# Kernel optimization log

Hardware: AMD Instinct MI355X
Metric: run time of the kernel (lower is better)

Reference implementation:

```python
import jax, jax.numpy as jnp
import numpy as np

D = 512; H = 8; DH = 64; FF = 2048; NL = 4
CB = 8; V = 2048
NFFT = 1280; HOP = 320; WIN = 1280; SWIN = 30; UP = 6
B = 2; T = 256


def setup_inputs() -> dict:
    key = jax.random.key(0)
    ks = jax.random.split(key, 12)
    s = 0.02
    return {
        "codes": jax.random.randint(ks[0], (B, CB, T), 0, V),
        "emb": jax.random.normal(ks[1], (CB * V, D), jnp.float32) * s,
        "ln1": jnp.ones((NL, D), jnp.float32),
        "ln2": jnp.ones((NL, D), jnp.float32),
        "fln": jnp.ones((D,), jnp.float32),
        "wq": jax.random.normal(ks[2], (NL, D, D), jnp.float32) * s,
        "wk": jax.random.normal(ks[3], (NL, D, D), jnp.float32) * s,
        "wv": jax.random.normal(ks[4], (NL, D, D), jnp.float32) * s,
        "wo": jax.random.normal(ks[5], (NL, D, D), jnp.float32) * s,
        "wg": jax.random.normal(ks[6], (NL, D, FF), jnp.float32) * s,
        "wu": jax.random.normal(ks[7], (NL, D, FF), jnp.float32) * s,
        "wd": jax.random.normal(ks[8], (NL, FF, D), jnp.float32) * s,
        "lin_w": jax.random.normal(ks[9], (D, 1282), jnp.float32) * s,
        "lin_b": jnp.zeros((1282,), jnp.float32),
    }


def _rmsnorm(x, w):
    return x * jax.lax.rsqrt(jnp.mean(x * x, axis=-1, keepdims=True) + 1e-5) * w


def _forward(codes, emb, ln1, ln2, fln, wq, wk, wv, wo, wg, wu, wd, lin_w, lin_b):
    b, c, t = codes.shape
    # FusedEmbedding: offset per codebook, lookup, mean over codebooks -> [B,T,D]
    ids = codes + (jnp.arange(c) * V)[None, :, None]
    x = emb[ids].mean(axis=1)
    x = jnp.repeat(x, UP, axis=1)  # [B,S,D]
    S = x.shape[1]
    idx = jnp.arange(S)
    d = idx[None, :] - idx[:, None]
    mask = (d <= 0) & (d > -SWIN)  # [S,S] causal sliding-window band
    scale = float(1.0 / np.sqrt(DH))
    for l in range(NL):
        h = _rmsnorm(x, ln1[l])
        q = (h @ wq[l]).reshape(b, S, H, DH)
        k = (h @ wk[l]).reshape(b, S, H, DH)
        v = (h @ wv[l]).reshape(b, S, H, DH)
        sc = jnp.einsum('bqhd,bkhd->bhqk', q, k) * scale
        sc = jnp.where(mask[None, None], sc, jnp.float32(-1e30))
        a = jax.nn.softmax(sc, axis=-1)
        o = jnp.einsum('bhqk,bkhd->bqhd', a, v).reshape(b, S, D) @ wo[l]
        x = x + o
        h = _rmsnorm(x, ln2[l])
        x = x + (jax.nn.silu(h @ wg[l]) * (h @ wu[l])) @ wd[l]
    x = _rmsnorm(x, fln)
    x = x @ lin_w + lin_b            # [B,S,1282]
    x = jnp.swapaxes(x, 1, 2)        # [B,1282,S]
    log_abs, angle = jnp.split(x, 2, axis=1)  # [B,641,S] each
    mag = jnp.exp(log_abs)
    spec = jax.lax.complex(mag * jnp.cos(angle), mag * jnp.sin(angle))
    # ISTFT with 'same' padding (Vocos-style overlap-add)
    ifft = jnp.fft.irfft(spec, n=NFFT, axis=1)               # [B,NFFT,S]
    n = jnp.arange(WIN, dtype=jnp.float32)
    win = 0.5 * (1.0 - jnp.cos(2.0 * jnp.pi * n / WIN))      # periodic hann
    ifft = ifft * win[None, :, None]
    out_size = (S - 1) * HOP + WIN
    pos = (jnp.arange(S)[:, None] * HOP + jnp.arange(WIN)[None, :]).reshape(-1)
    frames = jnp.swapaxes(ifft, 1, 2).reshape(b, -1)
    y = jnp.zeros((b, out_size), ifft.dtype).at[:, pos].add(frames)
    env = jnp.zeros((out_size,), jnp.float32).at[pos].add(jnp.tile(win * win, S))
    pad = (WIN - HOP) // 2
    return y[:, pad:-pad] / env[pad:-pad]


def reference(codes, emb, ln1, ln2, fln, wq, wk, wv, wo, wg, wu, wd, lin_w, lin_b):
    return _forward(codes, emb, ln1, ln2, fln, wq, wk, wv, wo, wg, wu, wd, lin_w, lin_b)
```

## Files before the change

### kernel.cpp

```cpp
#include <hip/hip_runtime.h>
#include <math.h>

#define B_    2
#define T_    256
#define S_    1536
#define D_    512
#define H_    8
#define DH_   64
#define FF_   2048
#define V_    2048
#define NL_   4
#define NFFT_ 1280
#define HOP_  320
#define WIN_  1280
#define NBIN_ 641
#define NC_   1282
#define NPADL 1344
#define PAD_  480
#define OUTL_ 491520
#define SWIN_ 30
#define ROW_  (B_ * S_)
#define NH_   641
#define KH_   704
#define NHP_  704

#define TWO_PI_OVER_N 0.004908738521234052f

typedef unsigned short ushort_t;
typedef __attribute__((ext_vector_type(8))) short short8;
typedef __attribute__((ext_vector_type(8))) unsigned short ushort8_t;
typedef __attribute__((ext_vector_type(4))) float f32x4;

__device__ __forceinline__ ushort_t f2bf(float x) {
    unsigned int u = __builtin_bit_cast(unsigned int, x);
    u = (u + 0x7fffu + ((u >> 16) & 1u)) >> 16;
    return (ushort_t)u;
}
__device__ __forceinline__ float bf2f(ushort_t h) {
    unsigned int u = ((unsigned int)h) << 16;
    return __builtin_bit_cast(float, u);
}

#define GLL16(gp, sp) \
    __builtin_amdgcn_global_load_lds((const __attribute__((address_space(1))) void*)(gp), \
                                     (__attribute__((address_space(3))) void*)(sp), 16, 0, 0)

__device__ __forceinline__ int soff64(int r) {
    return r * 128;
}

__global__ __launch_bounds__(256) void k_embed(const int* __restrict__ codes,
                                               const float* __restrict__ emb,
                                               float* __restrict__ X)
{
    int idx = blockIdx.x * 256 + threadIdx.x;
    int d  = idx & (D_ - 1);
    int bt = idx >> 9;
    int t  = bt & (T_ - 1);
    int b  = bt >> 8;
    float s = 0.f;
#pragma unroll
    for (int cb = 0; cb < 8; ++cb) {
        int code = codes[(b * 8 + cb) * T_ + t];
        s += emb[(size_t)(cb * V_ + code) * D_ + d];
    }
    s *= 0.125f;
    float* xp = X + (size_t)(b * S_ + t * 6) * D_ + d;
#pragma unroll
    for (int r = 0; r < 6; ++r) xp[(size_t)r * D_] = s;
}

__global__ __launch_bounds__(256) void k_rmsnorm(const float* __restrict__ X,
                                                 const float* __restrict__ w,
                                                 ushort_t* __restrict__ Hh,
                                                 ushort_t* __restrict__ Hl)
{
    int row = blockIdx.x;
    int tid = threadIdx.x;
    const float* x = X + (size_t)row * D_;
    float v0 = x[tid], v1 = x[tid + 256];
    float ss = v0 * v0 + v1 * v1;
#pragma unroll
    for (int m = 1; m < 64; m <<= 1) ss += __shfl_xor(ss, m);
    __shared__ float red[4];
    if ((tid & 63) == 0) red[tid >> 6] = ss;
    __syncthreads();
    float tot = red[0] + red[1] + red[2] + red[3];
    float sc = rsqrtf(tot * (1.f / (float)D_) + 1e-5f);
    float y0 = v0 * sc * w[tid];
    float y1 = v1 * sc * w[tid + 256];
    ushort_t h0 = f2bf(y0), h1 = f2bf(y1);
    Hh[(size_t)row * D_ + tid]       = h0;
    Hh[(size_t)row * D_ + tid + 256] = h1;
    if (Hl) {
        Hl[(size_t)row * D_ + tid]       = f2bf(y0 - bf2f(h0));
        Hl[(size_t)row * D_ + tid + 256] = f2bf(y1 - bf2f(h1));
    }
}

__global__ __launch_bounds__(256) void k_castT(const float* __restrict__ src,
                                               ushort_t* __restrict__ dh,
                                               ushort_t* __restrict__ dl,
                                               int K, int N,
                                               long srcBatchStride, long dstBatchStride)
{
    src += (size_t)blockIdx.z * srcBatchStride;
    dh  += (size_t)blockIdx.z * dstBatchStride;
    if (dl) dl += (size_t)blockIdx.z * dstBatchStride;
    __shared__ float t[32][33];
    int n0 = blockIdx.x * 32, k0 = blockIdx.y * 32;
    int tx = threadIdx.x & 31, ty = threadIdx.x >> 5;
#pragma unroll
    for (int i = 0; i < 4; ++i) {
        int k = k0 + ty + 8 * i, n = n0 + tx;
        t[ty + 8 * i][tx] = (n < N) ? src[(size_t)k * N + n] : 0.f;
    }
    __syncthreads();
#pragma unroll
    for (int i = 0; i < 4; ++i) {
        int n = n0 + ty + 8 * i;
        float v = t[tx][ty + 8 * i];
        ushort_t h = f2bf(v);
        dh[(size_t)n * K + k0 + tx] = h;
        if (dl) dl[(size_t)n * K + k0 + tx] = f2bf(v - bf2f(h));
    }
}

template<bool SPLIT, bool CBF16, bool HASRES, bool HASBIAS>
__global__ __launch_bounds__(256) void gemm_mfma(
    const ushort_t* __restrict__ Ah, const ushort_t* __restrict__ Al,
    const ushort_t* __restrict__ Bh, const ushort_t* __restrict__ Bl,
    const float* __restrict__ Res, const float* __restrict__ bias,
    float* __restrict__ Cf, ushort_t* __restrict__ Cb,
    int K, int Nstore, size_t az, size_t bz, size_t cz)
{
    const size_t zo = blockIdx.z;
    Ah += zo * az; Bh += zo * bz;
    if (SPLIT) { Al += zo * az; Bl += zo * bz; }
    if (CBF16) Cb += zo * cz; else Cf += zo * cz;

    const int f  = blockIdx.y * gridDim.x + blockIdx.x;
    const int tx = f / gridDim.y;
    const int ty = f - tx * gridDim.y;

    __shared__ __align__(16) ushort_t lds[SPLIT ? 16384 : 8192];
    ushort_t* AsH = lds;
    ushort_t* BsH = lds + 4096;

    const int tid  = threadIdx.x;
    const int wave = tid >> 6, lane = tid & 63;
    const int row0 = ty * 64;
    const int col0 = tx * 64;
    const int wr = (wave >> 1) * 32, wc = (wave & 1) * 32;

    const int sr0 = tid >> 3, js = tid & 7;
    const int sr1 = 32 + sr0;
    const int jg0 = (js - (sr0 >> 1)) & 7;
    const int jg1 = (js - (sr1 >> 1)) & 7;
    const size_t aSrc0 = (size_t)(row0 + sr0) * K + jg0 * 8;
    const size_t aSrc1 = (size_t)(row0 + sr1) * K + jg1 * 8;
    const size_t bSrc0 = (size_t)(col0 + sr0) * K + jg0 * 8;
    const size_t bSrc1 = (size_t)(col0 + sr1) * K + jg1 * 8;
    const int d0 = tid * 16, d1 = d0 + 4096;

    const int kg = lane >> 4;
    const int lr = lane & 15;
    const int rA0 = wr + lr,      rA1 = wr + 16 + lr;
    const int rB0 = wc + lr,      rB1 = wc + 16 + lr;
    const int offA0 = rA0 * 128 + (((kg + (rA0 >> 1)) & 7) * 16);
    const int offA1 = rA1 * 128 + (((kg + (rA1 >> 1)) & 7) * 16);
    const int offB0 = rB0 * 128 + (((kg + (rB0 >> 1)) & 7) * 16);
    const int offB1 = rB1 * 128 + (((kg + (rB1 >> 1)) & 7) * 16);

    f32x4 acc00 = {0.f,0.f,0.f,0.f}, acc01 = acc00, acc10 = acc00, acc11 = acc00;

    for (int k0 = 0; k0 < K; k0 += 64) {
        GLL16(Ah + aSrc0 + k0, (char*)AsH + d0);
        GLL16(Ah + aSrc1 + k0, (char*)AsH + d1);
        GLL16(Bh + bSrc0 + k0, (char*)BsH + d0);
        GLL16(Bh + bSrc1 + k0, (char*)BsH + d1);
        if constexpr (SPLIT) {
            GLL16(Al + aSrc0 + k0, (char*)(lds + 8192)  + d0);
            GLL16(Al + aSrc1 + k0, (char*)(lds + 8192)  + d1);
            GLL16(Bl + bSrc0 + k0, (char*)(lds + 12288) + d0);
            GLL16(Bl + bSrc1 + k0, (char*)(lds + 12288) + d1);
        }
        __syncthreads();
#pragma unroll
        for (int h = 0; h < 2; ++h) {
            const int hx = h * 64;
            short8 a0 = *(const short8*)((const char*)AsH + (offA0 ^ hx));
            short8 a1 = *(const short8*)((const char*)AsH + (offA1 ^ hx));
            short8 b0 = *(const short8*)((const char*)BsH + (offB0 ^ hx));
            short8 b1 = *(const short8*)((const char*)BsH + (offB1 ^ hx));
            acc00 = __builtin_amdgcn_mfma_f32_16x16x32_bf16(a0, b0, acc00, 0, 0, 0);
            acc01 = __builtin_amdgcn_mfma_f32_16x16x32_bf16(a0, b1, acc01, 0, 0, 0);
            acc10 = __builtin_amdgcn_mfma_f32_16x16x32_bf16(a1, b0, acc10, 0, 0, 0);
            acc11 = __builtin_amdgcn_mfma_f32_16x16x32_bf16(a1, b1, acc11, 0, 0, 0);
            if constexpr (SPLIT) {
                short8 al0 = *(const short8*)((const char*)(lds + 8192)  + (offA0 ^ hx));
                short8 al1 = *(const short8*)((const char*)(lds + 8192)  + (offA1 ^ hx));
                short8 bl0 = *(const short8*)((const char*)(lds + 12288) + (offB0 ^ hx));
                short8 bl1 = *(const short8*)((const char*)(lds + 12288) + (offB1 ^ hx));
                acc00 = __builtin_amdgcn_mfma_f32_16x16x32_bf16(a0, bl0, acc00, 0, 0, 0);
                acc00 = __builtin_amdgcn_mfma_f32_16x16x32_bf16(al0, b0, acc00, 0, 0, 0);
                acc01 = __builtin_amdgcn_mfma_f32_16x16x32_bf16(a0, bl1, acc01, 0, 0, 0);
                acc01 = __builtin_amdgcn_mfma_f32_16x16x32_bf16(al0, b1, acc01, 0, 0, 0);
                acc10 = __builtin_amdgcn_mfma_f32_16x16x32_bf16(a1, bl0, acc10, 0, 0, 0);
                acc10 = __builtin_amdgcn_mfma_f32_16x16x32_bf16(al1, b0, acc10, 0, 0, 0);
                acc11 = __builtin_amdgcn_mfma_f32_16x16x32_bf16(a1, bl1, acc11, 0, 0, 0);
                acc11 = __builtin_amdgcn_mfma_f32_16x16x32_bf16(al1, b1, acc11, 0, 0, 0);
            }
        }
        __syncthreads();
    }

    const int crow = row0 + wr + (lane >> 4) * 4;
    const int ccol = col0 + wc + lr;
#pragma unroll
    for (int i = 0; i < 2; ++i) {
#pragma unroll
        for (int j = 0; j < 2; ++j) {
            const f32x4 a = (i == 0) ? (j == 0 ? acc00 : acc01) : (j == 0 ? acc10 : acc11);
            int c = ccol + j * 16;
            if (c >= Nstore) continue;
            float bi = HASBIAS ? bias[c] : 0.f;
#pragma unroll
            for (int r = 0; r < 4; ++r) {
                int rr = crow + i * 16 + r;
                float v = a[r] + bi;
                if (HASRES) v += Res[(size_t)rr * Nstore + c];
                if (CBF16) Cb[(size_t)rr * Nstore + c] = f2bf(v);
                else       Cf[(size_t)rr * Nstore + c] = v;
            }
        }
    }
}

__global__ __launch_bounds__(256) void gemm_swiglu(
    const ushort_t* __restrict__ Ah,
    const ushort_t* __restrict__ Bg, const ushort_t* __restrict__ Bu,
    ushort_t* __restrict__ F, int K)
{
    const int f  = blockIdx.y * gridDim.x + blockIdx.x;
    const int tx = f / gridDim.y;
    const int ty = f - tx * gridDim.y;

    __shared__ __align__(16) ushort_t lds[12288];
    ushort_t* As  = lds;
    ushort_t* Bgs = lds + 4096;
    ushort_t* Bus = lds + 8192;

    const int tid  = threadIdx.x;
    const int wave = tid >> 6, lane = tid & 63;
    const int row0 = ty * 64;
    const int col0 = tx * 64;
    const int wr = (wave >> 1) * 32, wc = (wave & 1) * 32;

    const int sr0 = tid >> 3, js = tid & 7;
    const int sr1 = 32 + sr0;
    const int jg0 = (js - (sr0 >> 1)) & 7;
    const int jg1 = (js - (sr1 >> 1)) & 7;
    const size_t aSrc0 = (size_t)(row0 + sr0) * K + jg0 * 8;
    const size_t aSrc1 = (size_t)(row0 + sr1) * K + jg1 * 8;
    const size_t bSrc0 = (size_t)(col0 + sr0) * K + jg0 * 8;
    const size_t bSrc1 = (size_t)(col0 + sr1) * K + jg1 * 8;
    const int d0 = tid * 16, d1 = d0 + 4096;

    const int kg = lane >> 4;
    const int lr = lane & 15;
    const int rA0 = wr + lr,      rA1 = wr + 16 + lr;
    const int rB0 = wc + lr,      rB1 = wc + 16 + lr;
    const int offA0 = rA0 * 128 + (((kg + (rA0 >> 1)) & 7) * 16);
    const int offA1 = rA1 * 128 + (((kg + (rA1 >> 1)) & 7) * 16);
    const int offB0 = rB0 * 128 + (((kg + (rB0 >> 1)) & 7) * 16);
    const int offB1 = rB1 * 128 + (((kg + (rB1 >> 1)) & 7) * 16);

    f32x4 g00 = {0.f,0.f,0.f,0.f}, g01 = g00, g10 = g00, g11 = g00;
    f32x4 u00 = g00, u01 = g00, u10 = g00, u11 = g00;

    for (int k0 = 0; k0 < K; k0 += 64) {
        GLL16(Ah + aSrc0 + k0, (char*)As  + d0);
        GLL16(Ah + aSrc1 + k0, (char*)As  + d1);
        GLL16(Bg + bSrc0 + k0, (char*)Bgs + d0);
        GLL16(Bg + bSrc1 + k0, (char*)Bgs + d1);
        GLL16(Bu + bSrc0 + k0, (char*)Bus + d0);
        GLL16(Bu + bSrc1 + k0, (char*)Bus + d1);
        __syncthreads();
#pragma unroll
        for (int h = 0; h < 2; ++h) {
            const int hx = h * 64;
            short8 a0  = *(const short8*)((const char*)As  + (offA0 ^ hx));
            short8 a1  = *(const short8*)((const char*)As  + (offA1 ^ hx));
            short8 bg0 = *(const short8*)((const char*)Bgs + (offB0 ^ hx));
            short8 bg1 = *(const short8*)((const char*)Bgs + (offB1 ^ hx));
            short8 bu0 = *(const short8*)((const char*)Bus + (offB0 ^ hx));
            short8 bu1 = *(const short8*)((const char*)Bus + (offB1 ^ hx));
            g00 = __builtin_amdgcn_mfma_f32_16x16x32_bf16(a0, bg0, g00, 0, 0, 0);
            g01 = __builtin_amdgcn_mfma_f32_16x16x32_bf16(a0, bg1, g01, 0, 0, 0);
            g10 = __builtin_amdgcn_mfma_f32_16x16x32_bf16(a1, bg0, g10, 0, 0, 0);
            g11 = __builtin_amdgcn_mfma_f32_16x16x32_bf16(a1, bg1, g11, 0, 0, 0);
            u00 = __builtin_amdgcn_mfma_f32_16x16x32_bf16(a0, bu0, u00, 0, 0, 0);
            u01 = __builtin_amdgcn_mfma_f32_16x16x32_bf16(a0, bu1, u01, 0, 0, 0);
            u10 = __builtin_amdgcn_mfma_f32_16x16x32_bf16(a1, bu0, u10, 0, 0, 0);
            u11 = __builtin_amdgcn_mfma_f32_16x16x32_bf16(a1, bu1, u11, 0, 0, 0);
        }
        __syncthreads();
    }

    const int crow = row0 + wr + (lane >> 4) * 4;
    const int ccol = col0 + wc + lr;
#pragma unroll
    for (int i = 0; i < 2; ++i) {
#pragma unroll
        for (int j = 0; j < 2; ++j) {
            const f32x4 g = (i == 0) ? (j == 0 ? g00 : g01) : (j == 0 ? g10 : g11);
            const f32x4 u = (i == 0) ? (j == 0 ? u00 : u01) : (j == 0 ? u10 : u11);
            int c = ccol + j * 16;
#pragma unroll
            for (int r = 0; r < 4; ++r) {
                int rr = crow + i * 16 + r;
                float gv = g[r];
                float v = (gv / (1.f + expf(-gv))) * u[r];
                F[(size_t)rr * FF_ + c] = f2bf(v);
            }
        }
    }
}

__global__ __launch_bounds__(256) void k_attn(const ushort_t* __restrict__ QKV,
                                              ushort_t* __restrict__ O)
{
    const int wv   = threadIdx.x >> 6;
    const int lane = threadIdx.x & 63;
    const int qi = lane >> 3;
    const int dg = lane & 7;
    const int nqb = S_ / 32;
    int blk  = blockIdx.x;
    int qblk = blk % nqb;
    int bh   = blk / nqb;
    int hh = bh & 7, bb = bh >> 3;
    int qp = qblk * 32 + wv * 8 + qi;
    const ushort_t* base = QKV + (size_t)bb * S_ * 1536 + hh * 64 + dg * 8;

    float q[8];
    {
        ushort8_t qv = *(const ushort8_t*)(base + (size_t)qp * 1536);
#pragma unroll
        for (int d = 0; d < 8; ++d) q[d] = bf2f(qv[d]) * 0.125f;
    }

    float sc[SWIN_];
    float mx = -3.0e38f;
#pragma unroll
    for (int jj = 0; jj < SWIN_; ++jj) {
        int j = qp - (SWIN_ - 1) + jj;
        int jc = j < 0 ? 0 : j;
        ushort8_t kv = *(const ushort8_t*)(base + (size_t)jc * 1536 + 512);
        float p = 0.f;
#pragma unroll
        for (int d = 0; d < 8; ++d) p += q[d] * bf2f(kv[d]);
        p += __shfl_xor(p, 1);
        p += __shfl_xor(p, 2);
        p += __shfl_xor(p, 4);
        p = (j >= 0) ? p : -1e30f;
        sc[jj] = p;
        mx = fmaxf(mx, p);
    }
    float den = 0.f;
#pragma unroll
    for (int jj = 0; jj < SWIN_; ++jj) { sc[jj] = __expf(sc[jj] - mx); den += sc[jj]; }
    float inv = 1.f / den;

    float acc[8] = {0.f,0.f,0.f,0.f,0.f,0.f,0.f,0.f};
#pragma unroll
    for (int jj = 0; jj < SWIN_; ++jj) {
        int j = qp - (SWIN_ - 1) + jj;
        int jc = j < 0 ? 0 : j;
        ushort8_t vv = *(const ushort8_t*)(base + (size_t)jc * 1536 + 1024);
        float p = sc[jj];
#pragma unroll
        for (int d = 0; d < 8; ++d) acc[d] += p * bf2f(vv[d]);
    }
    ushort8_t ov;
#pragma unroll
    for (int d = 0; d < 8; ++d) ov[d] = f2bf(acc[d] * inv);
    *(ushort8_t*)(O + (size_t)(bb * S_ + qp) * 512 + hh * 64 + dg * 8) = ov;
}

__global__ __launch_bounds__(256) void k_specm(const float* __restrict__ Y,
                                               ushort_t* __restrict__ Yh,
                                               ushort_t* __restrict__ Mh)
{
    int idx = blockIdx.x * 256 + threadIdx.x;
    const int P1 = 2 * ROW_ * KH_;
    if (idx < P1) {
        int k  = idx % KH_;
        int rz = idx / KH_;
        int row = rz % ROW_;
        int z   = rz / ROW_;
        float v = 0.f;
        if (k < NBIN_) {
            float la = Y[(size_t)row * NC_ + k];
            float an = Y[(size_t)row * NC_ + NBIN_ + k];
            float sn, cs;
            sincosf(an, &sn, &cs);
            v = expf(la) * (z ? sn : cs);
        }
        Yh[idx] = f2bf(v);
    } else {
        idx -= P1;
        if (idx >= 2 * NHP_ * KH_) return;
        int k  = idx % KH_;
        int nz = idx / KH_;
        int n  = nz % NHP_;
        int z  = nz / NHP_;
        float val = 0.f;
        if (k < NBIN_ && n < NBIN_) {
            int kn = (k * n) % NFFT_;
            float ang = (float)kn * TWO_PI_OVER_N;
            float ck = (k == 0 || k == NBIN_ - 1) ? 1.f : 2.f;
            float win = 0.5f * (1.f - cosf((float)n * TWO_PI_OVER_N));
            float sn, cs;
            sincosf(ang, &sn, &cs);
            val = (z ? sn : cs) * ck * win * (1.f / (float)NFFT_);
        }
        Mh[idx] = f2bf(val);
    }
}

__global__ __launch_bounds__(256) void k_overlap(const float* __restrict__ F2,
                                                 float* __restrict__ out)
{
    int idx = blockIdx.x * 256 + threadIdx.x;
    if (idx >= B_ * OUTL_) return;
    int j = idx % OUTL_;
    int b = idx / OUTL_;
    int m = j + PAD_;
    int smax = m / HOP_;            if (smax > S_ - 1) smax = S_ - 1;
    int smin = (m - (WIN_ - HOP_)) / HOP_;
    if (smin < 0) smin = 0;
    const float* FS = F2 + (size_t)ROW_ * NH_;
    float acc = 0.f, env = 0.f;
    for (int s = smin; s <= smax; ++s) {
        int off = m - s * HOP_;
        size_t row = (size_t)(b * S_ + s) * NH_;
        float v;
        if (off < NBIN_) v = F2[row + off] - FS[row + off];
        else             v = F2[row + (NFFT_ - off)] + FS[row + (NFFT_ - off)];
        acc += v;
        float w = 0.5f * (1.f - cosf((float)off * TWO_PI_OVER_N));
        env += w * w;
    }
    out[idx] = acc / env;
}

extern "C" void kernel_launch(void* const* d_in, const int* in_sizes, int n_in,
                              void* d_out, int out_size, void* d_ws, size_t ws_size,
                              hipStream_t stream)
{
    (void)in_sizes; (void)n_in; (void)out_size; (void)ws_size;
    const int*   codes = (const int*)  d_in[0];
    const float* emb   = (const float*)d_in[1];
    const float* ln1   = (const float*)d_in[2];
    const float* ln2   = (const float*)d_in[3];
    const float* fln   = (const float*)d_in[4];
    const float* wq    = (const float*)d_in[5];
    const float* wk    = (const float*)d_in[6];
    const float* wv    = (const float*)d_in[7];
    const float* wo    = (const float*)d_in[8];
    const float* wg    = (const float*)d_in[9];
    const float* wu    = (const float*)d_in[10];
    const float* wd    = (const float*)d_in[11];
    const float* lin_w = (const float*)d_in[12];
    const float* lin_b = (const float*)d_in[13];
    float* out = (float*)d_out;
    float* ws  = (float*)d_ws;

    size_t o = 0;
    float*    X     = ws;                  o += (size_t)ROW_ * D_;
    ushort_t* QKVbf = (ushort_t*)(ws + o); o += (size_t)ROW_ * 1536 / 2;
    ushort_t* Hb    = (ushort_t*)(ws + o); o += (size_t)ROW_ * D_ / 2;
    float*    OFY   = ws + o;              o += (size_t)ROW_ * NC_;
    ushort_t* O     = (ushort_t*)OFY;
    ushort_t* F     = (ushort_t*)(OFY + (size_t)ROW_ * D_ / 2);
    float*    Yb    = OFY;
    float*    F2    = OFY;
    ushort_t* wqkvT = (ushort_t*)(ws + o); o += (size_t)NL_ * 1536 * D_ / 2;
    ushort_t* woT   = (ushort_t*)(ws + o); o += (size_t)NL_ * D_ * D_ / 2;
    ushort_t* M2_h  = wqkvT;
    ushort_t* wguT  = (ushort_t*)(ws + o); o += (size_t)NL_ * 4096 * D_ / 2;
    ushort_t* Ysp_h = wguT;
    ushort_t* wdT   = (ushort_t*)(ws + o); o += (size_t)NL_ * D_ * FF_ / 2;
    ushort_t* Hlo   = wdT;
    ushort_t* linTh = (ushort_t*)(ws + o); o += (size_t)NPADL * D_ / 2;
    ushort_t* linTl = (ushort_t*)(ws + o); o += (size_t)NPADL * D_ / 2;

    dim3 blk(256);

    k_embed<<<dim3((B_ * T_ * D_) / 256), blk, 0, stream>>>(codes, emb, X);

    k_castT<<<dim3(16, 16, NL_), blk, 0, stream>>>(wq, wqkvT,            nullptr, D_, D_, (long)D_*D_, (long)1536*D_);
    k_castT<<<dim3(16, 16, NL_), blk, 0, stream>>>(wk, wqkvT + 512*512,  nullptr, D_, D_, (long)D_*D_, (long)1536*D_);
    k_castT<<<dim3(16, 16, NL_), blk, 0, stream>>>(wv, wqkvT + 1024*512, nullptr, D_, D_, (long)D_*D_, (long)1536*D_);
    k_castT<<<dim3(16, 16, NL_), blk, 0, stream>>>(wo, woT,              nullptr, D_, D_, (long)D_*D_, (long)D_*D_);
    k_castT<<<dim3(64, 16, NL_), blk, 0, stream>>>(wg, wguT,             nullptr, D_, FF_, (long)D_*FF_, (long)4096*D_);
    k_castT<<<dim3(64, 16, NL_), blk, 0, stream>>>(wu, wguT + 2048*512,  nullptr, D_, FF_, (long)D_*FF_, (long)4096*D_);
    k_castT<<<dim3(16, 64, NL_), blk, 0, stream>>>(wd, wdT,              nullptr, FF_, D_, (long)FF_*D_, (long)D_*FF_);
    k_castT<<<dim3(NPADL/32, 16, 1), blk, 0, stream>>>(lin_w, linTh, linTl, D_, NC_, 0, 0);

    for (int l = 0; l < NL_; ++l) {
        k_rmsnorm<<<dim3(ROW_), blk, 0, stream>>>(X, ln1 + l * D_, Hb, nullptr);
        gemm_mfma<false,true,false,false><<<dim3(24, 48), blk, 0, stream>>>(
            Hb, nullptr, wqkvT + (size_t)l * 1536 * D_, nullptr,
            nullptr, nullptr, nullptr, QKVbf, D_, 1536, 0, 0, 0);
        k_attn<<<dim3(B_ * H_ * (S_ / 32)), blk, 0, stream>>>(QKVbf, O);
        gemm_mfma<false,false,true,false><<<dim3(8, 48), blk, 0, stream>>>(
            O, nullptr, woT + (size_t)l * D_ * D_, nullptr,
            X, nullptr, X, nullptr, D_, D_, 0, 0, 0);
        k_rmsnorm<<<dim3(ROW_), blk, 0, stream>>>(X, ln2 + l * D_, Hb, nullptr);
        gemm_swiglu<<<dim3(32, 48), blk, 0, stream>>>(
            Hb, wguT + (size_t)l * 4096 * D_, wguT + (size_t)l * 4096 * D_ + (size_t)2048 * D_, F, D_);
        gemm_mfma<false,false,true,false><<<dim3(8, 48), blk, 0, stream>>>(
            F, nullptr, wdT + (size_t)l * D_ * FF_, nullptr,
            X, nullptr, X, nullptr, FF_, D_, 0, 0, 0);
    }

    k_rmsnorm<<<dim3(ROW_), blk, 0, stream>>>(X, fln, Hb, Hlo);
    gemm_mfma<true,false,false,true><<<dim3(NPADL/64, 48), blk, 0, stream>>>(
        Hb, Hlo, linTh, linTl, nullptr, lin_b, Yb, nullptr, D_, NC_, 0, 0, 0);
    {
        int total = 2 * ROW_ * KH_ + 2 * NHP_ * KH_;
        k_specm<<<dim3((total + 255) / 256), blk, 0, stream>>>(Yb, Ysp_h, M2_h);
    }
    gemm_mfma<false,false,false,false><<<dim3(NHP_/64, 48, 2), blk, 0, stream>>>(
        Ysp_h, nullptr, M2_h, nullptr, nullptr, nullptr, F2, nullptr, KH_, NH_,
        (size_t)ROW_ * KH_, (size_t)NHP_ * KH_, (size_t)ROW_ * NH_);
    k_overlap<<<dim3((B_ * OUTL_ + 255) / 256), blk, 0, stream>>>(F2, out);
}
```

Measured before the change: 666.6 us.

## Widen GEMM tiles to 64x128 and split-K the down projection

Adds a 64x128-tile GEMM kernel and uses it for the QKV projection and the ISTFT matmul, and widens the SwiGLU gate/up kernel to 128 columns per block. The goal is more reuse of each A tile from LDS and fewer blocks. The down projection is split-K into two partial buffers, which the next RMSNorm sums back into the residual, so each block handles a shorter K loop and more blocks run. The costs are more LDS and registers per block, an extra partial buffer, and extra memory traffic in the RMSNorm.

```diff
diff --git a/kernel.cpp b/kernel.cpp
--- a/kernel.cpp
+++ b/kernel.cpp
@@ -22,7 +22,7 @@
 #define ROW_  (B_ * S_)
 #define NH_   641
 #define KH_   704
-#define NHP_  704
+#define NHP2_ 768
 
 #define TWO_PI_OVER_N 0.004908738521234052f
 
@@ -45,8 +45,8 @@
     __builtin_amdgcn_global_load_lds((const __attribute__((address_space(1))) void*)(gp), \
                                      (__attribute__((address_space(3))) void*)(sp), 16, 0, 0)
 
-__device__ __forceinline__ int soff64(int r) {
-    return r * 128;
+__device__ __forceinline__ int fragoff(int r, int kg) {
+    return r * 128 + (((kg + (r >> 1)) & 7) * 16);
 }
 
 __global__ __launch_bounds__(256) void k_embed(const int* __restrict__ codes,
@@ -70,15 +70,23 @@
     for (int r = 0; r < 6; ++r) xp[(size_t)r * D_] = s;
 }
 
-__global__ __launch_bounds__(256) void k_rmsnorm(const float* __restrict__ X,
+__global__ __launch_bounds__(256) void k_rmsnorm(float* __restrict__ X,
+                                                 const float* __restrict__ P0,
+                                                 const float* __restrict__ P1,
                                                  const float* __restrict__ w,
                                                  ushort_t* __restrict__ Hh,
                                                  ushort_t* __restrict__ Hl)
 {
     int row = blockIdx.x;
     int tid = threadIdx.x;
-    const float* x = X + (size_t)row * D_;
+    float* x = X + (size_t)row * D_;
     float v0 = x[tid], v1 = x[tid + 256];
+    if (P0) {
+        size_t b = (size_t)row * D_;
+        v0 += P0[b + tid] + P1[b + tid];
+        v1 += P0[b + tid + 256] + P1[b + tid + 256];
+        x[tid] = v0; x[tid + 256] = v1;
+    }
     float ss = v0 * v0 + v1 * v1;
 #pragma unroll
     for (int m = 1; m < 64; m <<= 1) ss += __shfl_xor(ss, m);
@@ -132,7 +140,7 @@
     const ushort_t* __restrict__ Bh, const ushort_t* __restrict__ Bl,
     const float* __restrict__ Res, const float* __restrict__ bias,
     float* __restrict__ Cf, ushort_t* __restrict__ Cb,
-    int K, int Nstore, size_t az, size_t bz, size_t cz)
+    int Kloop, int Kstride, int Nstore, size_t az, size_t bz, size_t cz)
 {
     const size_t zo = blockIdx.z;
     Ah += zo * az; Bh += zo * bz;
@@ -154,27 +162,23 @@
     const int wr = (wave >> 1) * 32, wc = (wave & 1) * 32;
 
     const int sr0 = tid >> 3, js = tid & 7;
-    const int sr1 = 32 + sr0;
-    const int jg0 = (js - (sr0 >> 1)) & 7;
-    const int jg1 = (js - (sr1 >> 1)) & 7;
-    const size_t aSrc0 = (size_t)(row0 + sr0) * K + jg0 * 8;
-    const size_t aSrc1 = (size_t)(row0 + sr1) * K + jg1 * 8;
-    const size_t bSrc0 = (size_t)(col0 + sr0) * K + jg0 * 8;
-    const size_t bSrc1 = (size_t)(col0 + sr1) * K + jg1 * 8;
+    const int jg  = (js - (sr0 >> 1)) & 7;
+    const size_t aSrc0 = (size_t)(row0 + sr0) * Kstride + jg * 8;
+    const size_t aSrc1 = (size_t)(row0 + 32 + sr0) * Kstride + jg * 8;
+    const size_t bSrc0 = (size_t)(col0 + sr0) * Kstride + jg * 8;
+    const size_t bSrc1 = (size_t)(col0 + 32 + sr0) * Kstride + jg * 8;
     const int d0 = tid * 16, d1 = d0 + 4096;
 
     const int kg = lane >> 4;
     const int lr = lane & 15;
-    const int rA0 = wr + lr,      rA1 = wr + 16 + lr;
-    const int rB0 = wc + lr,      rB1 = wc + 16 + lr;
-    const int offA0 = rA0 * 128 + (((kg + (rA0 >> 1)) & 7) * 16);
-    const int offA1 = rA1 * 128 + (((kg + (rA1 >> 1)) & 7) * 16);
-    const int offB0 = rB0 * 128 + (((kg + (rB0 >> 1)) & 7) * 16);
-    const int offB1 = rB1 * 128 + (((kg + (rB1 >> 1)) & 7) * 16);
+    const int offA0 = fragoff(wr + lr, kg);
+    const int offA1 = fragoff(wr + 16 + lr, kg);
+    const int offB0 = fragoff(wc + lr, kg);
+    const int offB1 = fragoff(wc + 16 + lr, kg);
 
     f32x4 acc00 = {0.f,0.f,0.f,0.f}, acc01 = acc00, acc10 = acc00, acc11 = acc00;
 
-    for (int k0 = 0; k0 < K; k0 += 64) {
+    for (int k0 = 0; k0 < Kloop; k0 += 64) {
         GLL16(Ah + aSrc0 + k0, (char*)AsH + d0);
         GLL16(Ah + aSrc1 + k0, (char*)AsH + d1);
         GLL16(Bh + bSrc0 + k0, (char*)BsH + d0);
@@ -237,6 +241,95 @@
     }
 }
 
+template<bool CBF16>
+__global__ __launch_bounds__(256) void gemm_wide(
+    const ushort_t* __restrict__ Ah, const ushort_t* __restrict__ Bh,
+    float* __restrict__ Cf, ushort_t* __restrict__ Cb,
+    int Kloop, int Kstride, int Nstore, size_t az, size_t bz, size_t cz)
+{
+    const size_t zo = blockIdx.z;
+    Ah += zo * az; Bh += zo * bz;
+    if (CBF16) Cb += zo * cz; else Cf += zo * cz;
+
+    const int f  = blockIdx.y * gridDim.x + blockIdx.x;
+    const int tx = f / gridDim.y;
+    const int ty = f - tx * gridDim.y;
+
+    __shared__ __align__(16) ushort_t lds[12288];
+    ushort_t* AsH = lds;
+    ushort_t* BsH = lds + 4096;
+
+    const int tid  = threadIdx.x;
+    const int wave = tid >> 6, lane = tid & 63;
+    const int row0 = ty * 64;
+    const int col0 = tx * 128;
+    const int wr  = (wave >> 1) * 32;
+    const int wcc = (wave & 1) * 64;
+
+    const int sr = tid >> 3, js = tid & 7;
+    const int jg = (js - (sr >> 1)) & 7;
+    const int d0 = tid * 16;
+
+    const int kg = lane >> 4;
+    const int lr = lane & 15;
+    const int offA0 = fragoff(wr + lr, kg);
+    const int offA1 = fragoff(wr + 16 + lr, kg);
+    int offB[4];
+#pragma unroll
+    for (int j = 0; j < 4; ++j) offB[j] = fragoff(wcc + 16 * j + lr, kg);
+
+    f32x4 acc[2][4];
+#pragma unroll
+    for (int i = 0; i < 2; ++i)
+#pragma unroll
+        for (int j = 0; j < 4; ++j) acc[i][j] = (f32x4){0.f,0.f,0.f,0.f};
+
+    for (int k0 = 0; k0 < Kloop; k0 += 64) {
+#pragma unroll
+        for (int p = 0; p < 2; ++p)
+            GLL16(Ah + (size_t)(row0 + p * 32 + sr) * Kstride + jg * 8 + k0,
+                  (char*)AsH + p * 4096 + d0);
+#pragma unroll
+        for (int p = 0; p < 4; ++p)
+            GLL16(Bh + (size_t)(col0 + p * 32 + sr) * Kstride + jg * 8 + k0,
+                  (char*)BsH + p * 4096 + d0);
+        __syncthreads();
+#pragma unroll
+        for (int h = 0; h < 2; ++h) {
+            const int hx = h * 64;
+            short8 a0 = *(const short8*)((const char*)AsH + (offA0 ^ hx));
+            short8 a1 = *(const short8*)((const char*)AsH + (offA1 ^ hx));
+            short8 b[4];
+#pragma unroll
+            for (int j = 0; j < 4; ++j)
+                b[j] = *(const short8*)((const char*)BsH + (offB[j] ^ hx));
+#pragma unroll
+            for (int j = 0; j < 4; ++j) {
+                acc[0][j] = __builtin_amdgcn_mfma_f32_16x16x32_bf16(a0, b[j], acc[0][j], 0, 0, 0);
+                acc[1][j] = __builtin_amdgcn_mfma_f32_16x16x32_bf16(a1, b[j], acc[1][j], 0, 0, 0);
+            }
+        }
+        __syncthreads();
+    }
+
+    const int crow = row0 + wr + (lane >> 4) * 4;
+    const int ccol = col0 + wcc + lr;
+#pragma unroll
+    for (int i = 0; i < 2; ++i) {
+#pragma unroll
+        for (int j = 0; j < 4; ++j) {
+            int c = ccol + j * 16;
+            if (c >= Nstore) continue;
+#pragma unroll
+            for (int r = 0; r < 4; ++r) {
+                int rr = crow + i * 16 + r;
+                if (CBF16) Cb[(size_t)rr * Nstore + c] = f2bf(acc[i][j][r]);
+                else       Cf[(size_t)rr * Nstore + c] = acc[i][j][r];
+            }
+        }
+    }
+}
+
 __global__ __launch_bounds__(256) void gemm_swiglu(
     const ushort_t* __restrict__ Ah,
     const ushort_t* __restrict__ Bg, const ushort_t* __restrict__ Bu,
@@ -246,82 +339,78 @@
     const int tx = f / gridDim.y;
     const int ty = f - tx * gridDim.y;
 
-    __shared__ __align__(16) ushort_t lds[12288];
-    ushort_t* As  = lds;
+    __shared__ __align__(16) ushort_t lds[20480];
+    ushort_t* AsH = lds;
     ushort_t* Bgs = lds + 4096;
-    ushort_t* Bus = lds + 8192;
+    ushort_t* Bus = lds + 12288;
 
     const int tid  = threadIdx.x;
     const int wave = tid >> 6, lane = tid & 63;
     const int row0 = ty * 64;
-    const int col0 = tx * 64;
-    const int wr = (wave >> 1) * 32, wc = (wave & 1) * 32;
-
-    const int sr0 = tid >> 3, js = tid & 7;
-    const int sr1 = 32 + sr0;
-    const int jg0 = (js - (sr0 >> 1)) & 7;
-    const int jg1 = (js - (sr1 >> 1)) & 7;
-    const size_t aSrc0 = (size_t)(row0 + sr0) * K + jg0 * 8;
-    const size_t aSrc1 = (size_t)(row0 + sr1) * K + jg1 * 8;
-    const size_t bSrc0 = (size_t)(col0 + sr0) * K + jg0 * 8;
-    const size_t bSrc1 = (size_t)(col0 + sr1) * K + jg1 * 8;
-    const int d0 = tid * 16, d1 = d0 + 4096;
+    const int col0 = tx * 128;
+    const int wr  = (wave >> 1) * 32;
+    const int wcc = (wave & 1) * 64;
+
+    const int sr = tid >> 3, js = tid & 7;
+    const int jg = (js - (sr >> 1)) & 7;
+    const int d0 = tid * 16;
 
     const int kg = lane >> 4;
     const int lr = lane & 15;
-    const int rA0 = wr + lr,      rA1 = wr + 16 + lr;
-    const int rB0 = wc + lr,      rB1 = wc + 16 + lr;
-    const int offA0 = rA0 * 128 + (((kg + (rA0 >> 1)) & 7) * 16);
-    const int offA1 = rA1 * 128 + (((kg + (rA1 >> 1)) & 7) * 16);
-    const int offB0 = rB0 * 128 + (((kg + (rB0 >> 1)) & 7) * 16);
-    const int offB1 = rB1 * 128 + (((kg + (rB1 >> 1)) & 7) * 16);
-
-    f32x4 g00 = {0.f,0.f,0.f,0.f}, g01 = g00, g10 = g00, g11 = g00;
-    f32x4 u00 = g00, u01 = g00, u10 = g00, u11 = g00;
+    const int offA0 = fragoff(wr + lr, kg);
+    const int offA1 = fragoff(wr + 16 + lr, kg);
+    int offB[4];
+#pragma unroll
+    for (int j = 0; j < 4; ++j) offB[j] = fragoff(wcc + 16 * j + lr, kg);
+
+    f32x4 g[2][4], u[2][4];
+#pragma unroll
+    for (int i = 0; i < 2; ++i)
+#pragma unroll
+        for (int j = 0; j < 4; ++j) { g[i][j] = (f32x4){0.f,0.f,0.f,0.f}; u[i][j] = g[i][j]; }
 
     for (int k0 = 0; k0 < K; k0 += 64) {
-        GLL16(Ah + aSrc0 + k0, (char*)As  + d0);
-        GLL16(Ah + aSrc1 + k0, (char*)As  + d1);
-        GLL16(Bg + bSrc0 + k0, (char*)Bgs + d0);
-        GLL16(Bg + bSrc1 + k0, (char*)Bgs + d1);
-        GLL16(Bu + bSrc0 + k0, (char*)Bus + d0);
-        GLL16(Bu + bSrc1 + k0, (char*)Bus + d1);
+#pragma unroll
+        for (int p = 0; p < 2; ++p)
+            GLL16(Ah + (size_t)(row0 + p * 32 + sr) * K + jg * 8 + k0,
+                  (char*)AsH + p * 4096 + d0);
+#pragma unroll
+        for (int p = 0; p < 4; ++p) {
+            const size_t src = (size_t)(col0 + p * 32 + sr) * K + jg * 8 + k0;
+            GLL16(Bg + src, (char*)Bgs + p * 4096 + d0);
+            GLL16(Bu + src, (char*)Bus + p * 4096 + d0);
+        }
         __syncthreads();
 #pragma unroll
         for (int h = 0; h < 2; ++h) {
             const int hx = h * 64;
-            short8 a0  = *(const short8*)((const char*)As  + (offA0 ^ hx));
-            short8 a1  = *(const short8*)((const char*)As  + (offA1 ^ hx));
-            short8 bg0 = *(const short8*)((const char*)Bgs + (offB0 ^ hx));
-            short8 bg1 = *(const short8*)((const char*)Bgs + (offB1 ^ hx));
-            short8 bu0 = *(const short8*)((const char*)Bus + (offB0 ^ hx));
-            short8 bu1 = *(const short8*)((const char*)Bus + (offB1 ^ hx));
-            g00 = __builtin_amdgcn_mfma_f32_16x16x32_bf16(a0, bg0, g00, 0, 0, 0);
-            g01 = __builtin_amdgcn_mfma_f32_16x16x32_bf16(a0, bg1, g01, 0, 0, 0);
-            g10 = __builtin_amdgcn_mfma_f32_16x16x32_bf16(a1, bg0, g10, 0, 0, 0);
-            g11 = __builtin_amdgcn_mfma_f32_16x16x32_bf16(a1, bg1, g11, 0, 0, 0);
-            u00 = __builtin_amdgcn_mfma_f32_16x16x32_bf16(a0, bu0, u00, 0, 0, 0);
-            u01 = __builtin_amdgcn_mfma_f32_16x16x32_bf16(a0, bu1, u01, 0, 0, 0);
-            u10 = __builtin_amdgcn_mfma_f32_16x16x32_bf16(a1, bu0, u10, 0, 0, 0);
-            u11 = __builtin_amdgcn_mfma_f32_16x16x32_bf16(a1, bu1, u11, 0, 0, 0);
+            short8 a0 = *(const short8*)((const char*)AsH + (offA0 ^ hx));
+            short8 a1 = *(const short8*)((const char*)AsH + (offA1 ^ hx));
+#pragma unroll
+            for (int j = 0; j < 4; ++j) {
+                short8 bgj = *(const short8*)((const char*)Bgs + (offB[j] ^ hx));
+                short8 buj = *(const short8*)((const char*)Bus + (offB[j] ^ hx));
+                g[0][j] = __builtin_amdgcn_mfma_f32_16x16x32_bf16(a0, bgj, g[0][j], 0, 0, 0);
+                g[1][j] = __builtin_amdgcn_mfma_f32_16x16x32_bf16(a1, bgj, g[1][j], 0, 0, 0);
+                u[0][j] = __builtin_amdgcn_mfma_f32_16x16x32_bf16(a0, buj, u[0][j], 0, 0, 0);
+                u[1][j] = __builtin_amdgcn_mfma_f32_16x16x32_bf16(a1, buj, u[1][j], 0, 0, 0);
+            }
         }
         __syncthreads();
     }
 
     const int crow = row0 + wr + (lane >> 4) * 4;
-    const int ccol = col0 + wc + lr;
+    const int ccol = col0 + wcc + lr;
 #pragma unroll
     for (int i = 0; i < 2; ++i) {
 #pragma unroll
-        for (int j = 0; j < 2; ++j) {
-            const f32x4 g = (i == 0) ? (j == 0 ? g00 : g01) : (j == 0 ? g10 : g11);
-            const f32x4 u = (i == 0) ? (j == 0 ? u00 : u01) : (j == 0 ? u10 : u11);
+        for (int j = 0; j < 4; ++j) {
             int c = ccol + j * 16;
 #pragma unroll
             for (int r = 0; r < 4; ++r) {
                 int rr = crow + i * 16 + r;
-                float gv = g[r];
-                float v = (gv / (1.f + expf(-gv))) * u[r];
+                float gv = g[i][j][r];
+                float v = (gv / (1.f + expf(-gv))) * u[i][j][r];
                 F[(size_t)rr * FF_ + c] = f2bf(v);
             }
         }
@@ -410,11 +499,11 @@
         Yh[idx] = f2bf(v);
     } else {
         idx -= P1;
-        if (idx >= 2 * NHP_ * KH_) return;
+        if (idx >= 2 * NHP2_ * KH_) return;
         int k  = idx % KH_;
         int nz = idx / KH_;
-        int n  = nz % NHP_;
-        int z  = nz / NHP_;
+        int n  = nz % NHP2_;
+        int z  = nz / NHP2_;
         float val = 0.f;
         if (k < NBIN_ && n < NBIN_) {
             int kn = (k * n) % NFFT_;
@@ -495,6 +584,7 @@
     ushort_t* Hlo   = wdT;
     ushort_t* linTh = (ushort_t*)(ws + o); o += (size_t)NPADL * D_ / 2;
     ushort_t* linTl = (ushort_t*)(ws + o); o += (size_t)NPADL * D_ / 2;
+    float*    Pp    = ws + o;              o += (size_t)2 * ROW_ * D_;
 
     dim3 blk(256);
 
@@ -510,31 +600,33 @@
     k_castT<<<dim3(NPADL/32, 16, 1), blk, 0, stream>>>(lin_w, linTh, linTl, D_, NC_, 0, 0);
 
     for (int l = 0; l < NL_; ++l) {
-        k_rmsnorm<<<dim3(ROW_), blk, 0, stream>>>(X, ln1 + l * D_, Hb, nullptr);
-        gemm_mfma<false,true,false,false><<<dim3(24, 48), blk, 0, stream>>>(
-            Hb, nullptr, wqkvT + (size_t)l * 1536 * D_, nullptr,
-            nullptr, nullptr, nullptr, QKVbf, D_, 1536, 0, 0, 0);
+        k_rmsnorm<<<dim3(ROW_), blk, 0, stream>>>(
+            X, (l == 0) ? nullptr : Pp, Pp + (size_t)ROW_ * D_, ln1 + l * D_, Hb, nullptr);
+        gemm_wide<true><<<dim3(12, 48), blk, 0, stream>>>(
+            Hb, wqkvT + (size_t)l * 1536 * D_, nullptr, QKVbf, D_, D_, 1536, 0, 0, 0);
         k_attn<<<dim3(B_ * H_ * (S_ / 32)), blk, 0, stream>>>(QKVbf, O);
         gemm_mfma<false,false,true,false><<<dim3(8, 48), blk, 0, stream>>>(
             O, nullptr, woT + (size_t)l * D_ * D_, nullptr,
-            X, nullptr, X, nullptr, D_, D_, 0, 0, 0);
-        k_rmsnorm<<<dim3(ROW_), blk, 0, stream>>>(X, ln2 + l * D_, Hb, nullptr);
-        gemm_swiglu<<<dim3(32, 48), blk, 0, stream>>>(
+            X, nullptr, X, nullptr, D_, D_, D_, 0, 0, 0);
+        k_rmsnorm<<<dim3(ROW_), blk, 0, stream>>>(X, nullptr, nullptr, ln2 + l * D_, Hb, nullptr);
+        gemm_swiglu<<<dim3(16, 48), blk, 0, stream>>>(
             Hb, wguT + (size_t)l * 4096 * D_, wguT + (size_t)l * 4096 * D_ + (size_t)2048 * D_, F, D_);
-        gemm_mfma<false,false,true,false><<<dim3(8, 48), blk, 0, stream>>>(
+        gemm_mfma<false,false,false,false><<<dim3(8, 48, 2), blk, 0, stream>>>(
             F, nullptr, wdT + (size_t)l * D_ * FF_, nullptr,
-            X, nullptr, X, nullptr, FF_, D_, 0, 0, 0);
-    }
-
-    k_rmsnorm<<<dim3(ROW_), blk, 0, stream>>>(X, fln, Hb, Hlo);
+            nullptr, nullptr, Pp, nullptr, FF_ / 2, FF_, D_,
+            (size_t)(FF_ / 2), (size_t)(FF_ / 2), (size_t)ROW_ * D_);
+    }
+
+    k_rmsnorm<<<dim3(ROW_), blk, 0, stream>>>(
+        X, Pp, Pp + (size_t)ROW_ * D_, fln, Hb, Hlo);
     gemm_mfma<true,false,false,true><<<dim3(NPADL/64, 48), blk, 0, stream>>>(
-        Hb, Hlo, linTh, linTl, nullptr, lin_b, Yb, nullptr, D_, NC_, 0, 0, 0);
+        Hb, Hlo, linTh, linTl, nullptr, lin_b, Yb, nullptr, D_, D_, NC_, 0, 0, 0);
     {
-        int total = 2 * ROW_ * KH_ + 2 * NHP_ * KH_;
+        int total = 2 * ROW_ * KH_ + 2 * NHP2_ * KH_;
         k_specm<<<dim3((total + 255) / 256), blk, 0, stream>>>(Yb, Ysp_h, M2_h);
     }
-    gemm_mfma<false,false,false,false><<<dim3(NHP_/64, 48, 2), blk, 0, stream>>>(
-        Ysp_h, nullptr, M2_h, nullptr, nullptr, nullptr, F2, nullptr, KH_, NH_,
-        (size_t)ROW_ * KH_, (size_t)NHP_ * KH_, (size_t)ROW_ * NH_);
+    gemm_wide<false><<<dim3(NHP2_/128, 48, 2), blk, 0, stream>>>(
+        Ysp_h, M2_h, F2, nullptr, KH_, KH_, NH_,
+        (size_t)ROW_ * KH_, (size_t)NHP2_ * KH_, (size_t)ROW_ * NH_);
     k_overlap<<<dim3((B_ * OUTL_ + 255) / 256), blk, 0, stream>>>(F2, out);
 }
```

New measurement: 667.6 us. No clear change (+0.1%).
